# Performance work log

Measured on AMD Instinct MI355X. Metric: run time of the kernel, lower is better.

## Reference

```python
import jax, jax.numpy as jnp
import numpy as np

SFREQ = 128.0
BANDS = {'alpha': (8, 12), 'beta': (12, 30), 'delta': (0.5, 4), 'gamma': (30, 45), 'theta': (4, 8)}


def _trapz(y, xf):
    # y: (..., F) jnp, xf: (F,) numpy constant
    dx = np.diff(xf).astype(np.float32)
    return jnp.sum((y[..., 1:] + y[..., :-1]) * (0.5 * dx), axis=-1)


def setup_inputs() -> dict:
    key = jax.random.key(0)
    x = jax.random.normal(key, (2048, 64, 512), dtype=jnp.float32)
    return {"x": x}


def reference(x):
    B, C, T = x.shape
    # ---------- time-domain moments ----------
    mean = jnp.mean(x, axis=-1)                       # (B, C)
    xc = x - mean[..., None]
    m2 = jnp.mean(xc * xc, axis=-1)
    m3 = jnp.mean(xc * xc * xc, axis=-1)
    m4 = jnp.mean(jnp.square(xc * xc), axis=-1)
    std = jnp.sqrt(m2)
    skew = m3 / jnp.power(m2, 1.5)                    # scipy.stats.skew (biased)
    kurt = m4 / (m2 * m2) - 3.0                       # Fisher kurtosis (biased)
    rms = jnp.sqrt(jnp.mean(x * x, axis=-1))

    nperseg = min(256, T)
    step = nperseg // 2
    nseg = (T - nperseg) // step + 1
    seg_idx = np.arange(nseg)[:, None] * step + np.arange(nperseg)  # (nseg, nperseg)
    segs = x[..., seg_idx]                                          # (B, C, nseg, nperseg)
    segs = segs - jnp.mean(segs, axis=-1, keepdims=True)
    n = np.arange(nperseg)
    win = (0.5 - 0.5 * np.cos(2.0 * np.pi * n / nperseg)).astype(np.float32)
    scale = np.float32(1.0 / (SFREQ * np.sum(win.astype(np.float64) ** 2)))
    spec = jnp.fft.rfft(segs * win, axis=-1)                        # (B, C, nseg, F)
    psd = (jnp.square(spec.real) + jnp.square(spec.imag)) * scale
    if nperseg % 2 == 0:
        psd = psd.at[..., 1:-1].multiply(2.0)
    else:
        psd = psd.at[..., 1:].multiply(2.0)
    psd = jnp.mean(psd, axis=-2)                                    # (B, C, F)
    freqs = np.fft.rfftfreq(nperseg, 1.0 / SFREQ)                   # (F,) constant

    total_power = _trapz(psd, freqs)
    feats = {'mean': mean, 'std': std, 'skew': skew, 'kurtosis': kurt, 'rms': rms}
    for name, (lo, hi) in BANDS.items():
        mask = (freqs >= lo) & (freqs <= hi)
        bp = _trapz(psd[..., mask], freqs[mask])
        feats[f'{name}_power'] = bp
        feats[f'{name}_relative'] = jnp.where(total_power > 1e-6, bp / total_power, 0.0)

    # ---------- histogram entropy (10 bins over [min, max], natural log) ----------
    xmin = jnp.min(x, axis=-1)
    xmax = jnp.max(x, axis=-1)
    width = xmax - xmin
    safe_w = jnp.where(width > 0, width, 1.0)
    t = (x - xmin[..., None]) / safe_w[..., None] * 10.0
    bi = jnp.clip(t.astype(jnp.int32), 0, 9)                        # (B, C, T)
    flat = bi.reshape(B * C, T) + (np.arange(B * C, dtype=np.int32) * 10)[:, None]
    counts = jnp.zeros(B * C * 10, jnp.float32).at[flat.reshape(-1)].add(1.0)
    p = counts.reshape(B, C, 10) / T
    ent = -jnp.sum(jnp.where(p > 0, p * jnp.log(p), 0.0), axis=-1)
    feats['entropy'] = ent

    # ---------- peak frequency ----------
    feats['peak_freq'] = jnp.asarray(freqs, jnp.float32)[jnp.argmax(psd, axis=-1)]

    # ---------- assemble in sorted-key order: sorted(f'ch{c}_{name}') ----------
    names = sorted(feats)                                           # 17 names
    per_ch = jnp.stack([feats[nm] for nm in names], axis=-1)        # (B, C, 17)
    ch_order = sorted(range(C), key=lambda i: f'ch{i}_')
    fv = per_ch[:, np.array(ch_order), :].reshape(B, C * len(names))

    # ---------- z-norm over batch ----------
    fv = (fv - jnp.mean(fv, axis=0)) / (jnp.std(fv, axis=0) + 1e-6)
    return fv
```

## Files before the change

kernel.cpp:

```cpp
#include <hip/hip_runtime.h>
#include <math.h>

#define NB 2048
#define NC 64
#define NF 17
#define NCOL (NC * NF)

__device__ __constant__ int POS[64] = {
   0, 11, 22, 33, 44, 55, 60, 61, 62, 63,
   1,  2,  3,  4,  5,  6,  7,  8,  9, 10,
  12, 13, 14, 15, 16, 17, 18, 19, 20, 21,
  23, 24, 25, 26, 27, 28, 29, 30, 31, 32,
  34, 35, 36, 37, 38, 39, 40, 41, 42, 43,
  45, 46, 47, 48, 49, 50, 51, 52, 53, 54,
  56, 57, 58, 59
};


__global__ void init_tables(float* __restrict__ win, float2* __restrict__ tw) {
    int t = threadIdx.x;
    double ang = (2.0 * 3.14159265358979323846 / 256.0) * (double)t;
    double cv = cos(ang), sv = sin(ang);
    win[t] = (float)(0.5 - 0.5 * cv);
    tw[t] = make_float2((float)cv, (float)sv);
}

template <bool HAS_TAB>
__global__ __launch_bounds__(256) void feat_kernel(
    const float* __restrict__ x,
    const float* __restrict__ gwin, const float2* __restrict__ gtw,
    float* __restrict__ out)
{
    __shared__ __align__(16) float winS[256];
    __shared__ float2 twS[256];
    __shared__ float2 tw16S[16];
    __shared__ __align__(16) float wmem[4 * 832];
    __shared__ unsigned histS[4][10];

    const int t = threadIdx.x;
    const int wid = t >> 6, l = t & 63;
    const int bc = (blockIdx.x << 2) + wid;
    const int b = bc >> 6, c = bc & 63;

    if (HAS_TAB) {
        winS[t] = gwin[t];
        twS[t] = gtw[t];
        if (t < 16) tw16S[t] = gtw[t << 4];
    } else {
        float ang = (float)t * (6.28318530717958647692f / 256.0f);
        float sv, cv;
        sincosf(ang, &sv, &cv);
        winS[t] = 0.5f - 0.5f * cv;
        twS[t] = make_float2(cv, sv);
        if (t < 16) {
            float a2 = (float)t * (6.28318530717958647692f / 16.0f);
            float s2v, c2v; sincosf(a2, &s2v, &c2v);
            tw16S[t] = make_float2(c2v, s2v);
        }
    }
    __syncthreads();

    float* vseg = &wmem[wid * 832];
    float2* T = reinterpret_cast<float2*>(&wmem[wid * 832 + 256]);
    unsigned* hist = histS[wid];

    const float4* xp4 = reinterpret_cast<const float4*>(x + (size_t)bc * 512);
    const float4 xa = xp4[2 * l], xb = xp4[2 * l + 1];
    float xe[8] = {xa.x, xa.y, xa.z, xa.w, xb.x, xb.y, xb.z, xb.w};

    float psum = 0.f, s2 = 0.f, mn = xe[0], mx = xe[0];
#pragma unroll
    for (int e = 0; e < 8; e++) {
        psum += xe[e];
        s2 = fmaf(xe[e], xe[e], s2);
        mn = fminf(mn, xe[e]);
        mx = fmaxf(mx, xe[e]);
    }
    float g = psum;
#pragma unroll
    for (int m = 1; m < 16; m <<= 1) g += __shfl_xor(g, m, 64);
    const float g0 = __shfl(g, 0, 64), g1 = __shfl(g, 16, 64),
                g2 = __shfl(g, 32, 64), g3 = __shfl(g, 48, 64);
    const float S1 = (g0 + g1) + (g2 + g3);
#pragma unroll
    for (int m = 1; m < 64; m <<= 1) {
        s2 += __shfl_xor(s2, m, 64);
        mn = fminf(mn, __shfl_xor(mn, m, 64));
        mx = fmaxf(mx, __shfl_xor(mx, m, 64));
    }
    const float mean = S1 * (1.0f / 512.0f);

    float c2 = 0.f, c3 = 0.f, c4 = 0.f;
#pragma unroll
    for (int e = 0; e < 8; e++) {
        float a = xe[e] - mean;
        float a2 = a * a;
        c2 += a2;
        c3 = fmaf(a2, a, c3);
        c4 = fmaf(a2, a2, c4);
    }
#pragma unroll
    for (int m = 1; m < 64; m <<= 1) {
        c2 += __shfl_xor(c2, m, 64);
        c3 += __shfl_xor(c3, m, 64);
        c4 += __shfl_xor(c4, m, 64);
    }
    const float m2 = c2 * (1.0f / 512.0f);
    const float m3 = c3 * (1.0f / 512.0f);
    const float m4 = c4 * (1.0f / 512.0f);
    const float stdv = sqrtf(m2);
    const float skew = m3 / (m2 * stdv);
    const float kurt = m4 / (m2 * m2) - 3.0f;
    const float rms = sqrtf(s2 * (1.0f / 512.0f));

    if (l < 10) hist[l] = 0u;
    {
        float wdt = mx - mn;
        float safew = (wdt > 0.0f) ? wdt : 1.0f;
#pragma unroll
        for (int e = 0; e < 8; e++) {
            int bi = (int)((xe[e] - mn) / safew * 10.0f);
            bi = bi < 0 ? 0 : (bi > 9 ? 9 : bi);
            atomicAdd(&hist[bi], 1u);
        }
    }
    float entterm;
    {
        float cnt = (l < 10) ? (float)hist[l] : 0.0f;
        float p = cnt * (1.0f / 512.0f);
        entterm = (p > 0.0f) ? p * logf(p) : 0.0f;
#pragma unroll
        for (int m = 1; m < 16; m <<= 1) entterm += __shfl_xor(entterm, m, 64);
    }
    const float ent = -entterm;

    const int rb = l >> 4, n0 = l & 15;
    float2 tv;
    tv = tw16S[rb];             const float2 w16q1 = make_float2(tv.x, -tv.y);
    tv = tw16S[(2 * rb) & 15];  const float2 w16q2 = make_float2(tv.x, -tv.y);
    tv = tw16S[(3 * rb) & 15];  const float2 w16q3 = make_float2(tv.x, -tv.y);
    tv = twS[(4 * l) & 255];    const float2 step4 = make_float2(tv.x, -tv.y);
    tv = twS[l];                const float2 wq1 = make_float2(tv.x, -tv.y);
    tv = twS[(2 * l) & 255];    const float2 wq2 = make_float2(tv.x, -tv.y);
    tv = twS[(3 * l) & 255];    const float2 wq3 = make_float2(tv.x, -tv.y);
    float car[4], cai[4];
#pragma unroll
    for (int a = 0; a < 4; a++) {
        int mm = (rb * a) & 3;
        car[a] = (mm == 0) ? 1.f : ((mm == 2) ? -1.f : 0.f);
        cai[a] = (mm == 1) ? -1.f : ((mm == 3) ? 1.f : 0.f);
    }

    float P1 = 0.f, P2 = 0.f, P128 = 0.f;
#pragma unroll
    for (int s = 0; s < 3; s++) {
        const float smean =
            ((s == 0) ? (g0 + g1) : (s == 1) ? (g1 + g2) : (g2 + g3)) * (1.0f / 256.0f);
        const int D = l - 16 * s;
        float alt = 0.f;
        if (D >= 0 && D < 32) {
            const float4 wA = reinterpret_cast<const float4*>(winS)[2 * D];
            const float4 wB = reinterpret_cast<const float4*>(winS)[2 * D + 1];
            float wv0 = wA.x * (xe[0] - smean);
            float wv1 = wA.y * (xe[1] - smean);
            float wv2 = wA.z * (xe[2] - smean);
            float wv3 = wA.w * (xe[3] - smean);
            float wv4 = wB.x * (xe[4] - smean);
            float wv5 = wB.y * (xe[5] - smean);
            float wv6 = wB.z * (xe[6] - smean);
            float wv7 = wB.w * (xe[7] - smean);
            reinterpret_cast<float4*>(vseg)[2 * D] = make_float4(wv0, wv1, wv2, wv3);
            reinterpret_cast<float4*>(vseg)[2 * D + 1] = make_float4(wv4, wv5, wv6, wv7);
            alt = ((wv0 - wv1) + (wv2 - wv3)) + ((wv4 - wv5) + (wv6 - wv7));
        }
#pragma unroll
        for (int m = 1; m < 64; m <<= 1) alt += __shfl_xor(alt, m, 64);
        P128 = fmaf(alt, alt, P128);

        float v[16];
#pragma unroll
        for (int n1 = 0; n1 < 16; n1++) v[n1] = vseg[16 * n1 + n0];
        float Dre[4], Dim[4];
#pragma unroll
        for (int q = 0; q < 4; q++) {
            float dr = v[q], di = 0.f;
#pragma unroll
            for (int a = 1; a < 4; a++) {
                float vv = v[4 * a + q];
                dr = fmaf(vv, car[a], dr);
                di = fmaf(vv, cai[a], di);
            }
            Dre[q] = dr; Dim[q] = di;
        }
        const float E0r = Dre[0], E0i = Dim[0];
        const float E1r = Dre[1] * w16q1.x - Dim[1] * w16q1.y;
        const float E1i = Dre[1] * w16q1.y + Dim[1] * w16q1.x;
        const float E2r = Dre[2] * w16q2.x - Dim[2] * w16q2.y;
        const float E2i = Dre[2] * w16q2.y + Dim[2] * w16q2.x;
        const float E3r = Dre[3] * w16q3.x - Dim[3] * w16q3.y;
        const float E3i = Dre[3] * w16q3.y + Dim[3] * w16q3.x;
        T[(rb +  0) * 18 + n0] = make_float2((E0r + E1r) + (E2r + E3r),
                                             (E0i + E1i) + (E2i + E3i));
        T[(rb +  4) * 18 + n0] = make_float2((E0r + E1i) - (E2r + E3i),
                                             (E0i - E1r) + (E3r - E2i));
        T[(rb +  8) * 18 + n0] = make_float2((E0r - E1r) + (E2r - E3r),
                                             (E0i - E1i) + (E2i - E3i));
        T[(rb + 12) * 18 + n0] = make_float2((E0r - E1i) - (E2r - E3i),
                                             (E0i + E1r) - (E2i + E3r));

        float2 cur = make_float2(1.f, 0.f);
        float G0r = 0, G0i = 0, G1r = 0, G1i = 0, G2r = 0, G2i = 0, G3r = 0, G3i = 0;
#pragma unroll
        for (int a = 0; a < 4; a++) {
            const float4 t01 = *reinterpret_cast<const float4*>(&T[n0 * 18 + 4 * a]);
            const float4 t23 = *reinterpret_cast<const float4*>(&T[n0 * 18 + 4 * a + 2]);
            G0r = fmaf(t01.x, cur.x, fmaf(-t01.y, cur.y, G0r));
            G0i = fmaf(t01.x, cur.y, fmaf( t01.y, cur.x, G0i));
            G1r = fmaf(t01.z, cur.x, fmaf(-t01.w, cur.y, G1r));
            G1i = fmaf(t01.z, cur.y, fmaf( t01.w, cur.x, G1i));
            G2r = fmaf(t23.x, cur.x, fmaf(-t23.y, cur.y, G2r));
            G2i = fmaf(t23.x, cur.y, fmaf( t23.y, cur.x, G2i));
            G3r = fmaf(t23.z, cur.x, fmaf(-t23.w, cur.y, G3r));
            G3i = fmaf(t23.z, cur.y, fmaf( t23.w, cur.x, G3i));
            if (a < 3) {
                float nx = cur.x * step4.x - cur.y * step4.y;
                float ny = cur.x * step4.y + cur.y * step4.x;
                cur = make_float2(nx, ny);
            }
        }
        const float H0r = G0r, H0i = G0i;
        const float H1r = G1r * wq1.x - G1i * wq1.y, H1i = G1r * wq1.y + G1i * wq1.x;
        const float H2r = G2r * wq2.x - G2i * wq2.y, H2i = G2r * wq2.y + G2i * wq2.x;
        const float H3r = G3r * wq3.x - G3i * wq3.y, H3i = G3r * wq3.y + G3i * wq3.x;
        const float X1r = (H0r + H1r) + (H2r + H3r);
        const float X1i = (H0i + H1i) + (H2i + H3i);
        const float X2r = (H0r + H1i) - (H2r + H3i);
        const float X2i = (H0i - H1r) + (H3r - H2i);
        P1 = fmaf(X1r, X1r, fmaf(X1i, X1i, P1));
        P2 = fmaf(X2r, X2r, fmaf(X2i, X2i, P2));
    }

    const float scc = (1.0f / 12288.0f) * (1.0f / 3.0f);
    const float psd1 = P1 * ((l == 0) ? 1.0f : 2.0f) * scc;
    const float psd2 = P2 * 2.0f * scc;
    const float psd128 = P128 * scc;

    auto wt = [](int k, int lo, int hi) -> float {
        if (k < lo || k > hi) return 0.0f;
        return (k == lo || k == hi) ? 0.25f : 0.5f;
    };
    float tot, al, be, de, ga, th, bv; int bi_;
    {
        const int k = l; const float p = psd1;
        tot = wt(k, 0, 128) * p;
        al = wt(k, 16, 24) * p; be = wt(k, 24, 60) * p; de = wt(k, 1, 8) * p;
        ga = wt(k, 60, 90) * p; th = wt(k, 8, 16) * p;
        bv = p; bi_ = k;
    }
    {
        const int k = l + 64; const float p = psd2;
        tot += 0.5f * p;
        ga += wt(k, 60, 90) * p;
        if (p > bv) { bv = p; bi_ = k; }
    }
    if (l == 0) {
        tot += 0.25f * psd128;
        if (psd128 > bv) { bv = psd128; bi_ = 128; }
    }
#pragma unroll
    for (int m = 1; m < 64; m <<= 1) {
        tot += __shfl_xor(tot, m, 64);
        al  += __shfl_xor(al, m, 64);
        be  += __shfl_xor(be, m, 64);
        de  += __shfl_xor(de, m, 64);
        ga  += __shfl_xor(ga, m, 64);
        th  += __shfl_xor(th, m, 64);
        float ov = __shfl_xor(bv, m, 64);
        int   oi = __shfl_xor(bi_, m, 64);
        if (ov > bv || (ov == bv && oi < bi_)) { bv = ov; bi_ = oi; }
    }
    const bool ok = tot > 1e-6f;
    const float alR = ok ? al / tot : 0.f;
    const float beR = ok ? be / tot : 0.f;
    const float deR = ok ? de / tot : 0.f;
    const float gaR = ok ? ga / tot : 0.f;
    const float thR = ok ? th / tot : 0.f;
    const float pkf = 0.5f * (float)bi_;

    if (l < NF) {
        float fv =
            (l == 0)  ? al :
            (l == 1)  ? alR :
            (l == 2)  ? be :
            (l == 3)  ? beR :
            (l == 4)  ? de :
            (l == 5)  ? deR :
            (l == 6)  ? ent :
            (l == 7)  ? ga :
            (l == 8)  ? gaR :
            (l == 9)  ? kurt :
            (l == 10) ? mean :
            (l == 11) ? pkf :
            (l == 12) ? rms :
            (l == 13) ? skew :
            (l == 14) ? stdv :
            (l == 15) ? th : thR;
        out[(size_t)b * NCOL + POS[c] * NF + l] = fv;
    }
}

__global__ __launch_bounds__(256) void znorm_kernel(float* __restrict__ fm) {
    __shared__ float red[4];
    const int col = blockIdx.x;
    const int t = threadIdx.x;
    const int wid = t >> 6, lane = t & 63;
    float v[8];
    float s = 0.0f;
#pragma unroll
    for (int i = 0; i < 8; i++) {
        v[i] = fm[(size_t)(i * 256 + t) * NCOL + col];
        s += v[i];
    }
#pragma unroll
    for (int off = 32; off; off >>= 1) s += __shfl_down(s, off, 64);
    if (lane == 0) red[wid] = s;
    __syncthreads();
    const float mu = (red[0] + red[1] + red[2] + red[3]) * (1.0f / 2048.0f);
    __syncthreads();
    float q = 0.0f;
#pragma unroll
    for (int i = 0; i < 8; i++) {
        float dd = v[i] - mu;
        q += dd * dd;
    }
#pragma unroll
    for (int off = 32; off; off >>= 1) q += __shfl_down(q, off, 64);
    if (lane == 0) red[wid] = q;
    __syncthreads();
    const float sd = sqrtf((red[0] + red[1] + red[2] + red[3]) * (1.0f / 2048.0f));
    const float den = sd + 1e-6f;
#pragma unroll
    for (int i = 0; i < 8; i++)
        fm[(size_t)(i * 256 + t) * NCOL + col] = (v[i] - mu) / den;
}

extern "C" void kernel_launch(void* const* d_in, const int* in_sizes, int n_in,
                              void* d_out, int out_size, void* d_ws, size_t ws_size,
                              hipStream_t stream) {
    const float* x = (const float*)d_in[0];
    float* out = (float*)d_out;
    const int nblocks = (NB * NC) / 4;
    if (d_ws != nullptr && ws_size >= 4096) {
        float* win = (float*)d_ws;
        float2* tw = (float2*)((char*)d_ws + 1024);
        init_tables<<<1, 256, 0, stream>>>(win, tw);
        feat_kernel<true><<<nblocks, 256, 0, stream>>>(x, win, tw, out);
    } else {
        feat_kernel<false><<<nblocks, 256, 0, stream>>>(x, nullptr, nullptr, out);
    }
    znorm_kernel<<<NCOL, 256, 0, stream>>>(out);
}
```

Before: 650.6 us.

## Split z-norm into coalesced partial-stats, finalize, and apply kernels

```diff
diff --git a/kernel.cpp b/kernel.cpp
--- a/kernel.cpp
+++ b/kernel.cpp
@@ -5,6 +5,12 @@
 #define NC 64
 #define NF 17
 #define NCOL (NC * NF)
+
+#define ZPB 16
+#define ZNB (NB / ZPB)
+#define WS_STATS_OFF 4096
+#define WS_PART_OFF 16384
+#define WS_FAST_BYTES (WS_PART_OFF + ZNB * NCOL * 8)
 
 __device__ __constant__ int POS[64] = {
    0, 11, 22, 33, 44, 55, 60, 61, 62, 63,
@@ -309,6 +315,62 @@
     }
 }
 
+
+__global__ __launch_bounds__(256) void zstat_partial(
+    const float* __restrict__ fm, float2* __restrict__ part)
+{
+    const int blk = blockIdx.x;
+    const int row0 = blk * ZPB;
+    for (int c = threadIdx.x; c < NCOL; c += 256) {
+        float s = 0.f, ss = 0.f;
+#pragma unroll
+        for (int r = 0; r < ZPB; r++) {
+            float v = fm[(size_t)(row0 + r) * NCOL + c];
+            s += v;
+            ss = fmaf(v, v, ss);
+        }
+        part[(size_t)blk * NCOL + c] = make_float2(s, ss);
+    }
+}
+
+__global__ __launch_bounds__(256) void zstat_final(
+    const float2* __restrict__ part, float2* __restrict__ stats)
+{
+    const int c = blockIdx.x * 256 + threadIdx.x;
+    if (c >= NCOL) return;
+    double s = 0.0, ss = 0.0;
+    for (int b = 0; b < ZNB; b++) {
+        float2 p = part[(size_t)b * NCOL + c];
+        s += (double)p.x;
+        ss += (double)p.y;
+    }
+    const double mu_d = s * (1.0 / 2048.0);
+    double var_d = ss * (1.0 / 2048.0) - mu_d * mu_d;
+    if (var_d < 0.0) var_d = 0.0;
+    const float mu = (float)mu_d;
+    const float sd = sqrtf((float)var_d);
+    stats[c] = make_float2(mu, sd + 1e-6f);
+}
+
+__global__ __launch_bounds__(256) void zapply(
+    float* __restrict__ fm, const float2* __restrict__ stats)
+{
+    const int row = blockIdx.x;
+    float4* p4 = reinterpret_cast<float4*>(fm + (size_t)row * NCOL);
+    for (int i = threadIdx.x; i < NCOL / 4; i += 256) {
+        float4 v = p4[i];
+        const float2 s0 = stats[4 * i + 0];
+        const float2 s1 = stats[4 * i + 1];
+        const float2 s2 = stats[4 * i + 2];
+        const float2 s3 = stats[4 * i + 3];
+        v.x = (v.x - s0.x) / s0.y;
+        v.y = (v.y - s1.x) / s1.y;
+        v.z = (v.z - s2.x) / s2.y;
+        v.w = (v.w - s3.x) / s3.y;
+        p4[i] = v;
+    }
+}
+
 __global__ __launch_bounds__(256) void znorm_kernel(float* __restrict__ fm) {
     __shared__ float red[4];
     const int col = blockIdx.x;
@@ -350,7 +412,11 @@
     const float* x = (const float*)d_in[0];
     float* out = (float*)d_out;
     const int nblocks = (NB * NC) / 4;
-    if (d_ws != nullptr && ws_size >= 4096) {
+
+    const bool has_tab = (d_ws != nullptr && ws_size >= 4096);
+    const bool fast_z = (d_ws != nullptr && ws_size >= (size_t)WS_FAST_BYTES);
+
+    if (has_tab) {
         float* win = (float*)d_ws;
         float2* tw = (float2*)((char*)d_ws + 1024);
         init_tables<<<1, 256, 0, stream>>>(win, tw);
@@ -358,5 +424,14 @@
     } else {
         feat_kernel<false><<<nblocks, 256, 0, stream>>>(x, nullptr, nullptr, out);
     }
-    znorm_kernel<<<NCOL, 256, 0, stream>>>(out);
-}
+
+    if (fast_z) {
+        float2* stats = (float2*)((char*)d_ws + WS_STATS_OFF);
+        float2* part = (float2*)((char*)d_ws + WS_PART_OFF);
+        zstat_partial<<<ZNB, 256, 0, stream>>>(out, part);
+        zstat_final<<<(NCOL + 255) / 256, 256, 0, stream>>>(part, stats);
+        zapply<<<NB, 256, 0, stream>>>(out, stats);
+    } else {
+        znorm_kernel<<<NCOL, 256, 0, stream>>>(out);
+    }
+}
```

New measurement: 629.1 us. 3.3% less time.
